# Optimization experiments

Hardware: AMD Instinct MI355X
Metric: run time of the kernel (lower is better)

Reference implementation:

```python
import jax, jax.numpy as jnp
import numpy as np
import math

L, B, T, C, H, DH, V, MEM = 6, 2, 1024, 1024, 16, 64, 32000, 128

def _ln(x, g, b):
    m = jnp.mean(x, -1, keepdims=True)
    v = jnp.mean((x - m) ** 2, -1, keepdims=True)
    return (x - m) * jax.lax.rsqrt(v + 1e-5) * g + b

def _rel_shift(x):
    # x: [B,H,Q,K]; TransformerXL shift trick: pad zero col, reshape, drop first row
    b, h, q, k = x.shape
    xp = jnp.pad(x, ((0, 0), (0, 0), (0, 0), (1, 0)))
    xp = xp.reshape(b, h, k + 1, q)
    return xp[:, :, 1:, :].reshape(b, h, q, k)

def setup_inputs():
    key = jax.random.key(0)
    ks = jax.random.split(key, 12)
    d = {}
    d['idx'] = jax.random.randint(ks[0], (B, T), 0, V)
    d['mems'] = jax.random.normal(ks[1], (L, B, MEM, C), dtype=jnp.float32) * 0.02
    d['wte'] = jax.random.normal(ks[2], (V, C), dtype=jnp.float32) * 0.02
    d['ln1_g'] = jnp.ones((L, C), jnp.float32); d['ln1_b'] = jnp.zeros((L, C), jnp.float32)
    d['attn_w'] = jax.random.normal(ks[3], (L, C, 3 * C), dtype=jnp.float32) * 0.02
    d['attn_b'] = jnp.zeros((L, 3 * C), jnp.float32)
    d['proj_w'] = jax.random.normal(ks[4], (L, C, C), dtype=jnp.float32) * 0.02
    d['proj_b'] = jnp.zeros((L, C), jnp.float32)
    d['r_emb'] = jax.random.normal(ks[5], (L, H, DH), dtype=jnp.float32) * 0.02
    d['r_bias'] = jax.random.normal(ks[6], (L, H, DH), dtype=jnp.float32) * 0.02
    d['ln2_g'] = jnp.ones((L, C), jnp.float32); d['ln2_b'] = jnp.zeros((L, C), jnp.float32)
    d['fc_w'] = jax.random.normal(ks[7], (L, C, 4 * C), dtype=jnp.float32) * 0.02
    d['fc_b'] = jnp.zeros((L, 4 * C), jnp.float32)
    d['fc2_w'] = jax.random.normal(ks[8], (L, 4 * C, C), dtype=jnp.float32) * 0.02
    d['fc2_b'] = jnp.zeros((L, C), jnp.float32)
    d['lnf_g'] = jnp.ones((C,), jnp.float32); d['lnf_b'] = jnp.zeros((C,), jnp.float32)
    d['lm_w'] = jax.random.normal(ks[9], (C, V), dtype=jnp.float32) * 0.02
    return d

def _attn(x, mem, w, b, pw, pb, remb, rbias):
    Bx, Tx, Cx = x.shape
    cat = jnp.concatenate([mem, x], axis=1)          # [B,K,C], K = mem_len + Tx
    K = cat.shape[1]
    qkv = cat @ w + b
    q, k, v = jnp.split(qkv, 3, axis=-1)
    q = q.reshape(Bx, K, H, DH).transpose(0, 2, 1, 3)
    k = k.reshape(Bx, K, H, DH).transpose(0, 2, 1, 3)
    v = v.reshape(Bx, K, H, DH).transpose(0, 2, 1, 3)
    q = q + rbias[None, :, None, :]
    AC = jnp.einsum('bhid,bhjd->bhij', q, k)
    # BD: r is r_emb broadcast over positions, so q@r^T is constant over j
    s = jnp.einsum('bhid,hd->bhi', q, remb)
    BD = _rel_shift(jnp.broadcast_to(s[..., None], (Bx, H, K, K)))
    p = jax.nn.softmax((AC + BD) / math.sqrt(DH), axis=-1)
    y = jnp.einsum('bhij,bhjd->bhid', p, v).transpose(0, 2, 1, 3).reshape(Bx, K, Cx)
    y = y @ pw + pb
    new_mem = cat[:, -MEM:]
    return y, new_mem

def reference(idx, mems, wte, ln1_g, ln1_b, attn_w, attn_b, proj_w, proj_b, r_emb, r_bias, ln2_g, ln2_b, fc_w, fc_b, fc2_w, fc2_b, lnf_g, lnf_b, lm_w):
    x = wte[idx]                                      # [B,T,C]
    new_mems = []
    for l in range(L):
        h = _ln(x, ln1_g[l], ln1_b[l])
        y, nm = _attn(h, mems[l], attn_w[l], attn_b[l], proj_w[l], proj_b[l], r_emb[l], r_bias[l])
        h2 = _ln(y, ln2_g[l], ln2_b[l])
        m = jax.nn.gelu(h2 @ fc_w[l] + fc_b[l], approximate=False) @ fc2_w[l] + fc2_b[l]
        x = y + m                                     # note: residual onto attn output (length grows by MEM per layer)
        new_mems.append(nm)
    x = _ln(x, lnf_g, lnf_b)
    logits = x @ lm_w                                 # [B, L*MEM+T, V]
    return logits, jnp.stack(new_mems)
```

## Files before the change

kernel.cpp:

```cpp
#include <hip/hip_runtime.h>
#include <hip/hip_bf16.h>
#include <hip/hip_fp16.h>

#define LNUM 6
#define BB 2
#define TT 1024
#define CC 1024
#define HH 16
#define DHH 64
#define VV 32000
#define MM 128

typedef _Float16 f16;
typedef _Float16 f16x8 __attribute__((ext_vector_type(8)));
typedef float f32x4 __attribute__((ext_vector_type(4)));

__device__ __forceinline__ void g2lds16(const void* g, void* l) {
    __builtin_amdgcn_global_load_lds((const __attribute__((address_space(1))) void*)g,
                                     (__attribute__((address_space(3))) void*)l,
                                     16, 0, 0);
}

__device__ __forceinline__ float wred(float v) {
#pragma unroll
    for (int o = 32; o > 0; o >>= 1) v += __shfl_xor(v, o);
    return v;
}

__global__ __launch_bounds__(256)
void transpose_k(const float* __restrict__ W, f16* __restrict__ WT, int R, int Cc)
{
    __shared__ float tile[64][65];
    const size_t base = (size_t)blockIdx.z * R * Cc;
    const int c0 = blockIdx.x * 64, r0 = blockIdx.y * 64;
    const int tx = threadIdx.x & 15, ty = threadIdx.x >> 4;
#pragma unroll
    for (int i = 0; i < 4; ++i) {
        const int row = ty + i * 16;
        float4 v = *(const float4*)&W[base + (size_t)(r0 + row) * Cc + c0 + tx * 4];
        tile[row][tx * 4 + 0] = v.x;
        tile[row][tx * 4 + 1] = v.y;
        tile[row][tx * 4 + 2] = v.z;
        tile[row][tx * 4 + 3] = v.w;
    }
    __syncthreads();
#pragma unroll
    for (int i = 0; i < 4; ++i) {
        const int c = ty + i * 16;
        union { f16 h4[4]; uint2 u; } pk;
        pk.h4[0] = (f16)tile[tx * 4 + 0][c];
        pk.h4[1] = (f16)tile[tx * 4 + 1][c];
        pk.h4[2] = (f16)tile[tx * 4 + 2][c];
        pk.h4[3] = (f16)tile[tx * 4 + 3][c];
        *(uint2*)&WT[base + (size_t)(c0 + c) * R + r0 + tx * 4] = pk.u;
    }
}

__global__ __launch_bounds__(256)
void embed_k(const int* __restrict__ idx, const float* __restrict__ wte, float* __restrict__ X)
{
    const int row = blockIdx.x;
    const int id = idx[row];
    const float4* src = (const float4*)(wte + (size_t)id * CC);
    float4* dst = (float4*)(X + (size_t)row * CC);
    dst[threadIdx.x] = src[threadIdx.x];
}

__global__ __launch_bounds__(256)
void ln_k(const float* __restrict__ X, const float* __restrict__ g,
          const float* __restrict__ bta, f16* __restrict__ outH)
{
    const int row = blockIdx.x * 4 + (threadIdx.x >> 6);
    const int lane = threadIdx.x & 63;
    const float4* xr = (const float4*)(X + (size_t)row * CC);
    float4 v[4];
    float s = 0.f;
#pragma unroll
    for (int i = 0; i < 4; ++i) { v[i] = xr[i * 64 + lane]; s += v[i].x + v[i].y + v[i].z + v[i].w; }
    s = wred(s);
    const float mean = s * (1.f / CC);
    float q = 0.f;
#pragma unroll
    for (int i = 0; i < 4; ++i) {
        float a = v[i].x - mean, b = v[i].y - mean, c = v[i].z - mean, d = v[i].w - mean;
        q += a * a + b * b + c * c + d * d;
    }
    q = wred(q);
    const float rs = rsqrtf(q * (1.f / CC) + 1e-5f);
    const float4* g4 = (const float4*)g;
    const float4* b4 = (const float4*)bta;
    uint2* orow = (uint2*)(outH + (size_t)row * CC);
#pragma unroll
    for (int i = 0; i < 4; ++i) {
        float4 gg = g4[i * 64 + lane], bb = b4[i * 64 + lane];
        union { f16 h4[4]; uint2 u; } pk;
        pk.h4[0] = (f16)((v[i].x - mean) * rs * gg.x + bb.x);
        pk.h4[1] = (f16)((v[i].y - mean) * rs * gg.y + bb.y);
        pk.h4[2] = (f16)((v[i].z - mean) * rs * gg.z + bb.z);
        pk.h4[3] = (f16)((v[i].w - mean) * rs * gg.w + bb.w);
        orow[i * 64 + lane] = pk.u;
    }
}

__global__ __launch_bounds__(256)
void ln1cat_k(const float* __restrict__ X, const float* __restrict__ memsL,
              const float* __restrict__ g, const float* __restrict__ bta,
              f16* __restrict__ catH, float* __restrict__ nmOut,
              int K, int Kin)
{
    const int row = blockIdx.x * 4 + (threadIdx.x >> 6);
    const int lane = threadIdx.x & 63;
    const int b = row / K, rr = row % K;
    uint2* crow = (uint2*)(catH + (size_t)row * CC);
    if (rr < MM) {
        const float4* src = (const float4*)(memsL + ((size_t)b * MM + rr) * CC);
#pragma unroll
        for (int i = 0; i < 4; ++i) {
            float4 vv = src[i * 64 + lane];
            union { f16 h4[4]; uint2 u; } pk;
            pk.h4[0] = (f16)vv.x; pk.h4[1] = (f16)vv.y; pk.h4[2] = (f16)vv.z; pk.h4[3] = (f16)vv.w;
            crow[i * 64 + lane] = pk.u;
        }
        return;
    }
    const float4* xr = (const float4*)(X + ((size_t)b * Kin + (rr - MM)) * CC);
    float4 v[4];
    float s = 0.f;
#pragma unroll
    for (int i = 0; i < 4; ++i) { v[i] = xr[i * 64 + lane]; s += v[i].x + v[i].y + v[i].z + v[i].w; }
    s = wred(s);
    const float mean = s * (1.f / CC);
    float q = 0.f;
#pragma unroll
    for (int i = 0; i < 4; ++i) {
        float a = v[i].x - mean, b2 = v[i].y - mean, c = v[i].z - mean, d = v[i].w - mean;
        q += a * a + b2 * b2 + c * c + d * d;
    }
    q = wred(q);
    const float rs = rsqrtf(q * (1.f / CC) + 1e-5f);
    const float4* g4 = (const float4*)g;
    const float4* b4 = (const float4*)bta;
    float4* nm = nullptr;
    if (rr >= K - MM) nm = (float4*)(nmOut + ((size_t)b * MM + (rr - (K - MM))) * CC);
#pragma unroll
    for (int i = 0; i < 4; ++i) {
        float4 gg = g4[i * 64 + lane], bb = b4[i * 64 + lane];
        float4 o;
        o.x = (v[i].x - mean) * rs * gg.x + bb.x;
        o.y = (v[i].y - mean) * rs * gg.y + bb.y;
        o.z = (v[i].z - mean) * rs * gg.z + bb.z;
        o.w = (v[i].w - mean) * rs * gg.w + bb.w;
        union { f16 h4[4]; uint2 u; } pk;
        pk.h4[0] = (f16)o.x; pk.h4[1] = (f16)o.y; pk.h4[2] = (f16)o.z; pk.h4[3] = (f16)o.w;
        crow[i * 64 + lane] = pk.u;
        if (nm) nm[i * 64 + lane] = o;
    }
}

template <int EPI>
__global__ __launch_bounds__(256, 2)
void gemm_k(const f16* __restrict__ A, const f16* __restrict__ BT,
            const float* __restrict__ bias, const float* __restrict__ res,
            float* __restrict__ outF, f16* __restrict__ outH,
            int M, int N, int Kc)
{
    __shared__ f16 sA[2][128 * 64];
    __shared__ f16 sB[2][128 * 64];

    const int nbn = N >> 7;
    const int nwg = gridDim.x;
    const int id = blockIdx.x;
    const int qq = nwg >> 3, r8 = nwg & 7;
    const int xcd = id & 7, pos = id >> 3;
    const int wgid = (xcd < r8 ? xcd * (qq + 1) : r8 * (qq + 1) + (xcd - r8) * qq) + pos;
    const int bm = wgid / nbn, bn = wgid % nbn;

    const int tid = threadIdx.x;
    const int w = tid >> 6, l = tid & 63;
    const int wr = w >> 1, wc = w & 1;
    const int lr = l & 15, lhi = l >> 4;

    f32x4 acc[4][4] = {};

    const f16* gA = A + (size_t)(bm * 128) * Kc;
    const f16* gB = BT + (size_t)(bn * 128) * Kc;

    auto stage = [&](int slot, int kt) {
#pragma unroll
        for (int p = 0; p < 4; ++p) {
            const int s = p * 256 + tid;
            const int row = s >> 3, gr = s & 7;
            const int srcoff = (gr ^ (row & 7)) << 3;
            g2lds16(gA + (size_t)row * Kc + kt + srcoff, &sA[slot][s * 8]);
            g2lds16(gB + (size_t)row * Kc + kt + srcoff, &sB[slot][s * 8]);
        }
    };

    stage(0, 0);
    asm volatile("s_waitcnt vmcnt(0)" ::: "memory");
    __builtin_amdgcn_s_barrier();

    int cur = 0;
    for (int kt = 0; kt < Kc; kt += 64) {
        if (kt + 64 < Kc) stage(cur ^ 1, kt + 64);
        f16x8 af[4][2], bf[4][2];
#pragma unroll
        for (int mi = 0; mi < 4; ++mi)
#pragma unroll
            for (int ks = 0; ks < 2; ++ks) {
                const int r = wr * 64 + mi * 16 + lr;
                af[mi][ks] = *(const f16x8*)&sA[cur][r * 64 + ((((ks << 2) + lhi) ^ (r & 7)) << 3)];
            }
#pragma unroll
        for (int ni = 0; ni < 4; ++ni)
#pragma unroll
            for (int ks = 0; ks < 2; ++ks) {
                const int r = wc * 64 + ni * 16 + lr;
                bf[ni][ks] = *(const f16x8*)&sB[cur][r * 64 + ((((ks << 2) + lhi) ^ (r & 7)) << 3)];
            }
        asm volatile("s_waitcnt lgkmcnt(0)" ::: "memory");
        __builtin_amdgcn_sched_barrier(0);
#pragma unroll
        for (int mi = 0; mi < 4; ++mi)
#pragma unroll
            for (int ni = 0; ni < 4; ++ni)
#pragma unroll
                for (int ks = 0; ks < 2; ++ks)
                    acc[mi][ni] = __builtin_amdgcn_mfma_f32_16x16x32_f16(af[mi][ks], bf[ni][ks], acc[mi][ni], 0, 0, 0);
        asm volatile("s_waitcnt vmcnt(0)" ::: "memory");
        __builtin_amdgcn_s_barrier();
        cur ^= 1;
    }

    const int orow0 = bm * 128 + wr * 64 + (l >> 4) * 4;
    const int ocol0 = bn * 128 + wc * 64 + lr;
#pragma unroll
    for (int mi = 0; mi < 4; ++mi)
#pragma unroll
        for (int ni = 0; ni < 4; ++ni) {
            const int col = ocol0 + ni * 16;
            const float bv = (EPI >= 1) ? bias[col] : 0.f;
#pragma unroll
            for (int r = 0; r < 4; ++r) {
                const int row = orow0 + mi * 16 + r;
                float v = acc[mi][ni][r] + bv;
                if (EPI == 2) {
                    const float u = 1.5957691216057308f * (v + 0.044715f * v * v * v);
                    const float e = __expf(u);
                    v = v * e / (e + 1.f);
                    outH[(size_t)row * N + col] = (f16)v;
                } else if (EPI == 4) {
                    outH[(size_t)row * N + col] = (f16)v;
                } else if (EPI == 3) {
                    v += res[(size_t)row * N + col];
                    outF[(size_t)row * N + col] = v;
                } else {
                    outF[(size_t)row * N + col] = v;
                }
            }
        }
}

template <int EPI>
__global__ __launch_bounds__(512, 2)
void gemm256_k(const f16* __restrict__ A, const f16* __restrict__ BT,
               const float* __restrict__ bias,
               float* __restrict__ outF, f16* __restrict__ outH,
               int M, int N, int Kc)
{
    __shared__ char ldsbuf[131072];
    char* ldsA = ldsbuf;
    char* ldsB = ldsbuf + 65536;

    const int nbm = M >> 8;
    const int nwg = gridDim.x;
    int id = blockIdx.x;
    const int qq = nwg >> 3, rr8 = nwg & 7;
    const int xcd = id & 7, pos = id >> 3;
    const int wgid = (xcd < rr8 ? xcd * (qq + 1) : rr8 * (qq + 1) + (xcd - rr8) * qq) + pos;
    const int bm = wgid % nbm, bn = wgid / nbm;

    const int t_ = threadIdx.x;
    const int w = t_ >> 6, l = t_ & 63;
    const int wm = w >> 2, wn = w & 3;
    const int lr = l & 15, lhi = l >> 4;

    const f16* gA = A + (size_t)bm * 256 * Kc;
    const f16* gB = BT + (size_t)bn * 256 * Kc;

    auto stage = [&](const f16* Gbase, char* ldsHalf, int kt) {
#pragma unroll
        for (int ii = 0; ii < 2; ++ii) {
            const int gb = (w << 1) + ii;
            const int s = (gb << 6) + l;
            const int row = s >> 3, grp = s & 7;
            g2lds16(Gbase + (size_t)row * Kc + kt + ((grp ^ (row & 7)) << 3),
                    ldsHalf + gb * 1024);
        }
    };
    auto rdfrag = [&](const char* halfBase, int rowInHalf, int ks) -> f16x8 {
        return *(const f16x8*)(halfBase + rowInHalf * 128 +
                               ((((ks << 2) + lhi) ^ (rowInHalf & 7)) << 4));
    };

    f32x4 acc[8][4] = {};
    f16x8 aA[4][2], blo[2][2], bhi[2][2];

    const int NT = Kc >> 6;
    const char* aHalf0 = ldsA + wm * 16384;
    const char* aHalf1 = ldsA + 32768 + wm * 16384;
    const char* bHalf0 = ldsB + (wn >> 1) * 16384;
    const char* bHalf1 = ldsB + 32768 + (wn >> 1) * 16384;
    const int brow = (wn & 1) * 64;

    stage(gA, ldsA + 0, 0);
    stage(gA + (size_t)128 * Kc, ldsA + 16384, 0);
    stage(gB, ldsB + 0, 0);
    stage(gB + (size_t)128 * Kc, ldsB + 16384, 0);
    stage(gB, ldsB + 32768, 64);
    stage(gB + (size_t)128 * Kc, ldsB + 49152, 64);
    asm volatile("s_waitcnt vmcnt(0)" ::: "memory");
    __builtin_amdgcn_s_barrier();

#define MFMA_QUAD(MQ, NQ, BR)                                                            \
    __builtin_amdgcn_s_setprio(1);                                                       \
    _Pragma("unroll") for (int mf = 0; mf < 4; ++mf)                                     \
    _Pragma("unroll") for (int nf = 0; nf < 2; ++nf)                                     \
    _Pragma("unroll") for (int ks = 0; ks < 2; ++ks)                                     \
        acc[(MQ)*4 + mf][(NQ)*2 + nf] =                                                  \
            __builtin_amdgcn_mfma_f32_16x16x32_f16(aA[mf][ks], BR[nf][ks],               \
                                                   acc[(MQ)*4 + mf][(NQ)*2 + nf], 0, 0, 0); \
    __builtin_amdgcn_s_setprio(0);

#define PHASE_SYNC()                                          \
    __builtin_amdgcn_s_barrier();                             \
    asm volatile("s_waitcnt lgkmcnt(0)" ::: "memory");        \
    __builtin_amdgcn_sched_barrier(0);

    for (int t = 0; t < NT; t += 2) {
        const bool pf0 = (t + 2) < NT;
        const int kb = (t + 1) << 6, kc2 = (t + 2) << 6, kd = (t + 3) << 6;

#pragma unroll
        for (int mf = 0; mf < 4; ++mf)
#pragma unroll
            for (int ks = 0; ks < 2; ++ks) aA[mf][ks] = rdfrag(aHalf0, mf * 16 + lr, ks);
#pragma unroll
        for (int nf = 0; nf < 2; ++nf)
#pragma unroll
            for (int ks = 0; ks < 2; ++ks) blo[nf][ks] = rdfrag(bHalf0, brow + nf * 16 + lr, ks);
        stage(gA, ldsA + 32768, kb);
        PHASE_SYNC();
        MFMA_QUAD(0, 0, blo);
        __builtin_amdgcn_s_barrier();

#pragma unroll
        for (int nf = 0; nf < 2; ++nf)
#pragma unroll
            for (int ks = 0; ks < 2; ++ks) bhi[nf][ks] = rdfrag(bHalf0, brow + 32 + nf * 16 + lr, ks);
        stage(gA + (size_t)128 * Kc, ldsA + 49152, kb);
        PHASE_SYNC();
        MFMA_QUAD(0, 1, bhi);
        __builtin_amdgcn_s_barrier();

#pragma unroll
        for (int mf = 0; mf < 4; ++mf)
#pragma unroll
            for (int ks = 0; ks < 2; ++ks) aA[mf][ks] = rdfrag(aHalf0, 64 + mf * 16 + lr, ks);
        if (pf0) stage(gB, ldsB + 0, kc2);
        PHASE_SYNC();
        MFMA_QUAD(1, 0, blo);
        __builtin_amdgcn_s_barrier();

        if (pf0) {
            stage(gB + (size_t)128 * Kc, ldsB + 16384, kc2);
            asm volatile("s_waitcnt vmcnt(4)" ::: "memory");
        } else {
            asm volatile("s_waitcnt vmcnt(0)" ::: "memory");
        }
        PHASE_SYNC();
        MFMA_QUAD(1, 1, bhi);
        __builtin_amdgcn_s_barrier();

#pragma unroll
        for (int mf = 0; mf < 4; ++mf)
#pragma unroll
            for (int ks = 0; ks < 2; ++ks) aA[mf][ks] = rdfrag(aHalf1, mf * 16 + lr, ks);
#pragma unroll
        for (int nf = 0; nf < 2; ++nf)
#pragma unroll
            for (int ks = 0; ks < 2; ++ks) blo[nf][ks] = rdfrag(bHalf1, brow + nf * 16 + lr, ks);
        if (pf0) stage(gA, ldsA + 0, kc2);
        PHASE_SYNC();
        MFMA_QUAD(0, 0, blo);
        __builtin_amdgcn_s_barrier();

#pragma unroll
        for (int nf = 0; nf < 2; ++nf)
#pragma unroll
            for (int ks = 0; ks < 2; ++ks) bhi[nf][ks] = rdfrag(bHalf1, brow + 32 + nf * 16 + lr, ks);
        if (pf0) stage(gA + (size_t)128 * Kc, ldsA + 16384, kc2);
        PHASE_SYNC();
        MFMA_QUAD(0, 1, bhi);
        __builtin_amdgcn_s_barrier();

#pragma unroll
        for (int mf = 0; mf < 4; ++mf)
#pragma unroll
            for (int ks = 0; ks < 2; ++ks) aA[mf][ks] = rdfrag(aHalf1, 64 + mf * 16 + lr, ks);
        if (pf0) stage(gB, ldsB + 32768, kd);
        PHASE_SYNC();
        MFMA_QUAD(1, 0, blo);
        __builtin_amdgcn_s_barrier();

        if (pf0) {
            stage(gB + (size_t)128 * Kc, ldsB + 49152, kd);
            asm volatile("s_waitcnt vmcnt(4)" ::: "memory");
        } else {
            asm volatile("s_waitcnt vmcnt(0)" ::: "memory");
        }
        PHASE_SYNC();
        MFMA_QUAD(1, 1, bhi);
        __builtin_amdgcn_s_barrier();
    }
#undef MFMA_QUAD
#undef PHASE_SYNC

    const int rb0 = bm * 256 + wm * 128 + lhi * 4;
    const int cb0 = bn * 256 + wn * 64 + lr;
#pragma unroll
    for (int mf = 0; mf < 8; ++mf)
#pragma unroll
        for (int nf = 0; nf < 4; ++nf) {
            const int col = cb0 + nf * 16;
            const float bv = (EPI >= 1) ? bias[col] : 0.f;
#pragma unroll
            for (int r = 0; r < 4; ++r) {
                const int row = rb0 + mf * 16 + r;
                float v = acc[mf][nf][r] + bv;
                if (EPI == 2) {
                    const float u = 1.5957691216057308f * (v + 0.044715f * v * v * v);
                    const float e = __expf(u);
                    v = v * e / (e + 1.f);
                    outH[(size_t)row * N + col] = (f16)v;
                } else if (EPI == 4) {
                    outH[(size_t)row * N + col] = (f16)v;
                } else {
                    outF[(size_t)row * N + col] = v;
                }
            }
        }
}

__global__ __launch_bounds__(256)
void attn_k(const f16* __restrict__ qkv, const float* __restrict__ remb,
            const float* __restrict__ rbias, f16* __restrict__ yH, int K)
{
    __shared__ f16 K_lds[2][64 * 64];
    __shared__ f16 Vt_lds[2][64 * 64];
    __shared__ f16 P_lds[64 * 64];
    __shared__ float s_s[66];

    const int b = blockIdx.x >> 4, h = blockIdx.x & 15;
    const int i0 = blockIdx.y * 64;
    const int t = threadIdx.x;
    const int w = t >> 6, l = t & 63;
    const int c = l & 15, g = l >> 4;

    const f16* qg = qkv + (size_t)b * K * 3072 + h * 64;
    const f16* kg = qg + 1024;
    const f16* vg = qg + 2048;
    const float* rb = rbias + h * 64;
    const float* re = remb + h * 64;

    const int kb = t >> 4, db = t & 15;

    auto stageK = [&](int j0, int slot) {
#pragma unroll
        for (int i = 0; i < 2; ++i) {
            const int s = w * 128 + i * 64 + l;
            const int row = s >> 3, grp = s & 7;
            g2lds16(kg + (size_t)(j0 + row) * 3072 + ((grp ^ (row & 7)) * 8),
                    (char*)K_lds[slot] + (size_t)(w * 128 + i * 64) * 16);
        }
    };
    auto loadV = [&](int j0, uint2* rowv) {
#pragma unroll
        for (int i = 0; i < 4; ++i)
            rowv[i] = *(const uint2*)(vg + (size_t)(j0 + kb * 4 + i) * 3072 + db * 4);
    };
    auto writeVt = [&](const uint2* rowvu, int slot) {
#pragma unroll
        for (int j = 0; j < 4; ++j) {
            union { uint2 u; f16 hh[4]; } colv;
#pragma unroll
            for (int i = 0; i < 4; ++i) {
                union { uint2 u; f16 hh[4]; } rv; rv.u = rowvu[i];
                colv.hh[i] = rv.hh[j];
            }
            const int d = db * 4 + j;
            *(uint2*)((char*)Vt_lds[slot] + d * 128 + ((kb * 8) ^ ((d & 7) << 4))) = colv.u;
        }
    };

    f16x8 qf[2];
    {
        const int qrow = i0 + w * 16 + c;
#pragma unroll
        for (int ks = 0; ks < 2; ++ks) {
            f16x8 raw = *(const f16x8*)(qg + (size_t)qrow * 3072 + ks * 32 + g * 8);
            f16x8 o;
#pragma unroll
            for (int j = 0; j < 8; ++j) o[j] = (f16)((float)raw[j] + rb[ks * 32 + g * 8 + j]);
            qf[ks] = o;
        }
    }
    if (t < 65) {
        float sv = 0.f;
        const int i = i0 + t;
        if (i < K) {
            const f16* qr = qg + (size_t)i * 3072;
#pragma unroll
            for (int d8 = 0; d8 < 8; ++d8) {
                f16x8 v8 = *(const f16x8*)(qr + d8 * 8);
#pragma unroll
                for (int j = 0; j < 8; ++j) sv += ((float)v8[j] + rb[d8 * 8 + j]) * re[d8 * 8 + j];
            }
        }
        s_s[t] = sv;
    }

    {
        uint2 rowv[4];
        stageK(0, 0);
        loadV(0, rowv);
        writeVt(rowv, 0);
    }
    __syncthreads();

    float sA[4], sB[4];
#pragma unroll
    for (int r = 0; r < 4; ++r) {
        sA[r] = s_s[w * 16 + g * 4 + r];
        sB[r] = s_s[w * 16 + g * 4 + r + 1];
    }

    float m_run[4] = {0.f, 0.f, 0.f, 0.f};
    float psum[4] = {0.f, 0.f, 0.f, 0.f};
    f32x4 yacc[4] = {};

    int cur = 0;
    for (int j0 = 0; j0 < K; j0 += 64, cur ^= 1) {
        const bool more = (j0 + 64) < K;
        uint2 rowv[4];
        if (more) { stageK(j0 + 64, cur ^ 1); loadV(j0 + 64, rowv); }

        f32x4 sc[4] = {};
#pragma unroll
        for (int tt = 0; tt < 4; ++tt) {
            const int row = tt * 16 + c;
#pragma unroll
            for (int ks = 0; ks < 2; ++ks) {
                f16x8 kf = *(const f16x8*)((char*)K_lds[cur] + row * 128 + ((ks * 64 + g * 16) ^ ((row & 7) << 4)));
                sc[tt] = __builtin_amdgcn_mfma_f32_16x16x32_f16(qf[ks], kf, sc[tt], 0, 0, 0);
            }
        }

        float p[4][4];
#pragma unroll
        for (int tt = 0; tt < 4; ++tt)
#pragma unroll
            for (int r = 0; r < 4; ++r) {
                const int gi = i0 + w * 16 + g * 4 + r;
                const int gj = j0 + tt * 16 + c;
                const float bd = (gj <= gi) ? sA[r] : ((gj == gi + 1) ? 0.f : sB[r]);
                p[tt][r] = (sc[tt][r] + bd) * 0.125f;
            }

        float lmax[4];
        bool need = false;
#pragma unroll
        for (int r = 0; r < 4; ++r) {
            lmax[r] = fmaxf(fmaxf(p[0][r], p[1][r]), fmaxf(p[2][r], p[3][r]));
            need |= (lmax[r] > m_run[r] + 8.f);
        }
        if (__any(need)) {
#pragma unroll
            for (int r = 0; r < 4; ++r) {
                float mx = lmax[r];
                mx = fmaxf(mx, __shfl_xor(mx, 1));
                mx = fmaxf(mx, __shfl_xor(mx, 2));
                mx = fmaxf(mx, __shfl_xor(mx, 4));
                mx = fmaxf(mx, __shfl_xor(mx, 8));
                if (mx > m_run[r]) {
                    const float f = __expf(m_run[r] - mx);
                    m_run[r] = mx;
                    psum[r] *= f;
#pragma unroll
                    for (int tt = 0; tt < 4; ++tt) yacc[tt][r] *= f;
                }
            }
        }
#pragma unroll
        for (int r = 0; r < 4; ++r) {
            float ss = 0.f;
#pragma unroll
            for (int tt = 0; tt < 4; ++tt) {
                const float e = __expf(p[tt][r] - m_run[r]);
                p[tt][r] = e;
                ss += e;
            }
            psum[r] += ss;
        }

        if (more) writeVt(rowv, cur ^ 1);
#pragma unroll
        for (int tt = 0; tt < 4; ++tt)
#pragma unroll
            for (int r = 0; r < 4; ++r) {
                const int q = w * 16 + g * 4 + r;
                *(f16*)((char*)P_lds + q * 128 + (((tt * 16 + c) * 2) ^ ((q & 7) << 4))) = (f16)p[tt][r];
            }
        asm volatile("s_waitcnt lgkmcnt(0)" ::: "memory");
        __builtin_amdgcn_sched_barrier(0);

        {
            const int qrow = w * 16 + c;
            f16x8 pa[2];
#pragma unroll
            for (int ks = 0; ks < 2; ++ks)
                pa[ks] = *(const f16x8*)((char*)P_lds + qrow * 128 + ((ks * 64 + g * 16) ^ ((qrow & 7) << 4)));
#pragma unroll
            for (int tt = 0; tt < 4; ++tt) {
                const int drow = tt * 16 + c;
#pragma unroll
                for (int ks = 0; ks < 2; ++ks) {
                    f16x8 vb = *(const f16x8*)((char*)Vt_lds[cur] + drow * 128 + ((ks * 64 + g * 16) ^ ((drow & 7) << 4)));
                    yacc[tt] = __builtin_amdgcn_mfma_f32_16x16x32_f16(pa[ks], vb, yacc[tt], 0, 0, 0);
                }
            }
        }
        __syncthreads();
    }

#pragma unroll
    for (int r = 0; r < 4; ++r) {
        float ps = psum[r];
        ps += __shfl_xor(ps, 1);
        ps += __shfl_xor(ps, 2);
        ps += __shfl_xor(ps, 4);
        ps += __shfl_xor(ps, 8);
        const float inv = 1.f / ps;
        const int row = i0 + w * 16 + g * 4 + r;
        f16* dst = yH + (size_t)(b * K + row) * CC + h * 64;
#pragma unroll
        for (int tt = 0; tt < 4; ++tt)
            dst[tt * 16 + c] = (f16)(yacc[tt][r] * inv);
    }
}

extern "C" void kernel_launch(void* const* d_in, const int* in_sizes, int n_in,
                              void* d_out, int out_size, void* d_ws, size_t ws_size,
                              hipStream_t stream)
{
    (void)in_sizes; (void)n_in; (void)out_size; (void)ws_size;
    const int*   idx    = (const int*)  d_in[0];
    const float* mems   = (const float*)d_in[1];
    const float* wte    = (const float*)d_in[2];
    const float* ln1_g  = (const float*)d_in[3];
    const float* ln1_b  = (const float*)d_in[4];
    const float* attn_w = (const float*)d_in[5];
    const float* attn_b = (const float*)d_in[6];
    const float* proj_w = (const float*)d_in[7];
    const float* proj_b = (const float*)d_in[8];
    const float* r_emb  = (const float*)d_in[9];
    const float* r_bias = (const float*)d_in[10];
    const float* ln2_g  = (const float*)d_in[11];
    const float* ln2_b  = (const float*)d_in[12];
    const float* fc_w   = (const float*)d_in[13];
    const float* fc_b   = (const float*)d_in[14];
    const float* fc2_w  = (const float*)d_in[15];
    const float* fc2_b  = (const float*)d_in[16];
    const float* lnf_g  = (const float*)d_in[17];
    const float* lnf_b  = (const float*)d_in[18];
    const float* lm_w   = (const float*)d_in[19];
    float* out = (float*)d_out;

    char* wp = (char*)d_ws; size_t off = 0;
    auto carve = [&](size_t bytes) -> void* {
        void* p = wp + off; off += (bytes + 255) & ~(size_t)255; return p;
    };
    const int KMAX = TT + LNUM * MM;
    f16*  attn_wT = (f16*) carve((size_t)LNUM * 3 * CC * CC * 2);
    f16*  proj_wT = (f16*) carve((size_t)LNUM * CC * CC * 2);
    f16*  fc_wT   = (f16*) carve((size_t)LNUM * 4 * CC * CC * 2);
    f16*  fc2_wT  = (f16*) carve((size_t)LNUM * 4 * CC * CC * 2);
    f16*  lm_wT   = (f16*) carve((size_t)VV * CC * 2);
    float* x0     = (float*)carve((size_t)BB * KMAX * CC * 4);
    float* x1     = (float*)carve((size_t)BB * KMAX * CC * 4);
    f16*  catH    = (f16*) carve((size_t)BB * KMAX * CC * 2);
    f16*  qkv16   = (f16*) carve((size_t)BB * KMAX * 3 * CC * 2);
    f16*  yH      = (f16*) carve((size_t)BB * KMAX * CC * 2);
    float* yp     = (float*)carve((size_t)BB * KMAX * CC * 4);
    f16*  h2H     = (f16*) carve((size_t)BB * KMAX * CC * 2);
    f16*  a1H     = (f16*) carve((size_t)BB * KMAX * 4 * CC * 2);
    f16*  xfH     = (f16*) carve((size_t)BB * KMAX * CC * 2);

    transpose_k<<<dim3(3 * CC / 64, CC / 64, LNUM), 256, 0, stream>>>(attn_w, attn_wT, CC, 3 * CC);
    transpose_k<<<dim3(CC / 64, CC / 64, LNUM),     256, 0, stream>>>(proj_w, proj_wT, CC, CC);
    transpose_k<<<dim3(4 * CC / 64, CC / 64, LNUM), 256, 0, stream>>>(fc_w, fc_wT, CC, 4 * CC);
    transpose_k<<<dim3(CC / 64, 4 * CC / 64, LNUM), 256, 0, stream>>>(fc2_w, fc2_wT, 4 * CC, CC);
    transpose_k<<<dim3(VV / 64, CC / 64, 1),        256, 0, stream>>>(lm_w, lm_wT, CC, VV);

    embed_k<<<BB * TT, 256, 0, stream>>>(idx, wte, x0);

    const size_t LOGITS = (size_t)BB * KMAX * VV;
    float* xcur = x0; float* xnxt = x1;
    for (int l = 0; l < LNUM; ++l) {
        const int Kin = TT + MM * l;
        const int K = Kin + MM;
        const int Mrows = BB * K;
        const int nbm128 = Mrows / 128;
        ln1cat_k<<<Mrows / 4, 256, 0, stream>>>(xcur, mems + (size_t)l * BB * MM * CC,
                                                ln1_g + l * CC, ln1_b + l * CC,
                                                catH, out + LOGITS + (size_t)l * BB * MM * CC, K, Kin);
        gemm_k<4><<<(3 * CC / 128) * nbm128, 256, 0, stream>>>(
            catH, attn_wT + (size_t)l * 3 * CC * CC, attn_b + (size_t)l * 3 * CC, nullptr,
            nullptr, qkv16, Mrows, 3 * CC, CC);
        attn_k<<<dim3(BB * HH, K / 64), 256, 0, stream>>>(
            qkv16, r_emb + (size_t)l * HH * DHH, r_bias + (size_t)l * HH * DHH, yH, K);
        gemm_k<1><<<(CC / 128) * nbm128, 256, 0, stream>>>(
            yH, proj_wT + (size_t)l * CC * CC, proj_b + (size_t)l * CC, nullptr,
            yp, nullptr, Mrows, CC, CC);
        ln_k<<<Mrows / 4, 256, 0, stream>>>(yp, ln2_g + l * CC, ln2_b + l * CC, h2H);
        gemm_k<2><<<(4 * CC / 128) * nbm128, 256, 0, stream>>>(
            h2H, fc_wT + (size_t)l * 4 * CC * CC, fc_b + (size_t)l * 4 * CC, nullptr,
            nullptr, a1H, Mrows, 4 * CC, CC);
        gemm_k<3><<<(CC / 128) * nbm128, 256, 0, stream>>>(
            a1H, fc2_wT + (size_t)l * 4 * CC * CC, fc2_b + (size_t)l * CC, yp,
            xnxt, nullptr, Mrows, CC, 4 * CC);
        float* tmp = xcur; xcur = xnxt; xnxt = tmp;
    }
    ln_k<<<(BB * KMAX) / 4, 256, 0, stream>>>(xcur, lnf_g, lnf_b, xfH);
    gemm256_k<0><<<(BB * KMAX / 256) * (VV / 256), 512, 0, stream>>>(
        xfH, lm_wT, nullptr, out, nullptr, BB * KMAX, VV, CC);
}
```

Before: 2.025 ms.

## Triple-buffer GEMM LDS with K-tile 32 and two-stage-ahead prefetch

The GEMM main loop moves from a double buffer with a K-tile of 64 to a triple buffer with a K-tile of 32. Loads are issued two tiles ahead, and a partial vmcnt wait lets the next tile's loads stay in flight while the current tile computes. The LDS layout becomes k-group-major with no XOR swizzle, and launch bounds go from 2 to 3 blocks per SM to raise occupancy. The cost is half as many MFMAs per barrier, which adds barrier and loop overhead. The unswizzled layout may also cause LDS bank conflicts.

```diff
diff --git a/kernel.cpp b/kernel.cpp
--- a/kernel.cpp
+++ b/kernel.cpp
@@ -158,14 +158,14 @@
 }
 
 template <int EPI>
-__global__ __launch_bounds__(256, 2)
+__global__ __launch_bounds__(256, 3)
 void gemm_k(const f16* __restrict__ A, const f16* __restrict__ BT,
             const float* __restrict__ bias, const float* __restrict__ res,
             float* __restrict__ outF, f16* __restrict__ outH,
             int M, int N, int Kc)
 {
-    __shared__ f16 sA[2][128 * 64];
-    __shared__ f16 sB[2][128 * 64];
+    __shared__ f16 sA[3][128 * 32];
+    __shared__ f16 sB[3][128 * 32];
 
     const int nbn = N >> 7;
     const int nwg = gridDim.x;
@@ -187,49 +187,47 @@
 
     auto stage = [&](int slot, int kt) {
 #pragma unroll
-        for (int p = 0; p < 4; ++p) {
-            const int s = p * 256 + tid;
-            const int row = s >> 3, gr = s & 7;
-            const int srcoff = (gr ^ (row & 7)) << 3;
-            g2lds16(gA + (size_t)row * Kc + kt + srcoff, &sA[slot][s * 8]);
-            g2lds16(gB + (size_t)row * Kc + kt + srcoff, &sB[slot][s * 8]);
+        for (int i = 0; i < 2; ++i) {
+            const int row = i * 64 + l;
+            g2lds16(gA + (size_t)row * Kc + kt + w * 8, &sA[slot][(w * 128 + row) * 8]);
+        }
+#pragma unroll
+        for (int i = 0; i < 2; ++i) {
+            const int row = i * 64 + l;
+            g2lds16(gB + (size_t)row * Kc + kt + w * 8, &sB[slot][(w * 128 + row) * 8]);
         }
     };
 
     stage(0, 0);
-    asm volatile("s_waitcnt vmcnt(0)" ::: "memory");
+    stage(1, 32);
+    asm volatile("s_waitcnt vmcnt(4)" ::: "memory");
     __builtin_amdgcn_s_barrier();
 
+    const int NT = Kc >> 5;
     int cur = 0;
-    for (int kt = 0; kt < Kc; kt += 64) {
-        if (kt + 64 < Kc) stage(cur ^ 1, kt + 64);
-        f16x8 af[4][2], bf[4][2];
+    for (int i = 0; i < NT; ++i) {
+        const int kt = i << 5;
+        const bool pf = (kt + 64) < Kc;
+        const int nxt2 = (cur + 2 >= 3) ? cur - 1 : cur + 2;
+        if (pf) stage(nxt2, kt + 64);
+        f16x8 af[4], bf[4];
 #pragma unroll
         for (int mi = 0; mi < 4; ++mi)
-#pragma unroll
-            for (int ks = 0; ks < 2; ++ks) {
-                const int r = wr * 64 + mi * 16 + lr;
-                af[mi][ks] = *(const f16x8*)&sA[cur][r * 64 + ((((ks << 2) + lhi) ^ (r & 7)) << 3)];
-            }
+            af[mi] = *(const f16x8*)&sA[cur][(lhi * 128 + wr * 64 + mi * 16 + lr) * 8];
 #pragma unroll
         for (int ni = 0; ni < 4; ++ni)
-#pragma unroll
-            for (int ks = 0; ks < 2; ++ks) {
-                const int r = wc * 64 + ni * 16 + lr;
-                bf[ni][ks] = *(const f16x8*)&sB[cur][r * 64 + ((((ks << 2) + lhi) ^ (r & 7)) << 3)];
-            }
+            bf[ni] = *(const f16x8*)&sB[cur][(lhi * 128 + wc * 64 + ni * 16 + lr) * 8];
         asm volatile("s_waitcnt lgkmcnt(0)" ::: "memory");
         __builtin_amdgcn_sched_barrier(0);
 #pragma unroll
         for (int mi = 0; mi < 4; ++mi)
 #pragma unroll
             for (int ni = 0; ni < 4; ++ni)
-#pragma unroll
-                for (int ks = 0; ks < 2; ++ks)
-                    acc[mi][ni] = __builtin_amdgcn_mfma_f32_16x16x32_f16(af[mi][ks], bf[ni][ks], acc[mi][ni], 0, 0, 0);
-        asm volatile("s_waitcnt vmcnt(0)" ::: "memory");
-        __builtin_amdgcn_s_barrier();
-        cur ^= 1;
+                acc[mi][ni] = __builtin_amdgcn_mfma_f32_16x16x32_f16(af[mi], bf[ni], acc[mi][ni], 0, 0, 0);
+        if (pf) { asm volatile("s_waitcnt vmcnt(4)" ::: "memory"); }
+        else    { asm volatile("s_waitcnt vmcnt(0)" ::: "memory"); }
+        __builtin_amdgcn_s_barrier();
+        cur = (cur + 1 >= 3) ? 0 : cur + 1;
     }
 
     const int orow0 = bm * 128 + wr * 64 + (l >> 4) * 4;
```

New measurement: 2.499 ms. 1.23x slower.
